# Kernel tuning notes

Measured on AMD Instinct MI355X. Metric: run time of the kernel, lower is better.

## Reference

```python
import jax, jax.numpy as jnp
import numpy as np

ROWS, COLS = 4096, 11008          # out_features, in_features
NCB, CBSIZE, CLEN = 2, 256, 8     # num_codebooks, 2**nbits, in_group_size
RANK = 32
BLOCK = ROWS                      # bolck_size = reference_weight.shape[0]
N_CODES = ROWS * COLS // CLEN     # total number of codebook entries gathered


def setup_inputs() -> dict:
    key = jax.random.key(0)
    k1, k2, k3, k4, k5 = jax.random.split(key, 5)
    codebooks = jax.random.normal(k1, (NCB, CBSIZE, CLEN), dtype=jnp.float32)
    codes = jax.random.randint(k2, (NCB, N_CODES // NCB), 0, CBSIZE, dtype=jnp.int32)
    scales = jax.random.uniform(k3, (COLS, 1), dtype=jnp.float32, minval=0.5, maxval=1.5)
    L = jax.random.normal(k4, (ROWS, RANK), dtype=jnp.float32) * 0.02
    R = jax.random.normal(k5, (RANK, COLS), dtype=jnp.float32) * 0.02
    return {"codebooks": codebooks, "codes": codes, "scales": scales, "L": L, "R": R}


def reference(codebooks, codes, scales, L, R):
    # differentiable_dequantize: per-codebook gather (embedding_bag with 1-elem
    # bags == plain gather), then per-block scale, then reshape back to weight.
    gathered = jax.vmap(lambda cb, c: cb[c])(codebooks, codes)  # (NCB, N/NCB, CLEN)
    blocks = gathered.reshape(-1, BLOCK) * scales               # (COLS, ROWS) * (COLS,1)
    dequant = blocks.reshape(ROWS, COLS)
    # low-rank correction
    return dequant + L @ R
```

## Files before the change

kernel.cpp:

```cpp
#include <hip/hip_runtime.h>

constexpr int kRows  = 4096;
constexpr int kCols  = 11008;
constexpr int kRank  = 32;

constexpr int RT    = 16;
constexpr int CT    = 256;
constexpr int PITCH = 260;

typedef __attribute__((ext_vector_type(8))) short short8;
typedef __attribute__((ext_vector_type(4))) float f32x4;

__device__ __forceinline__ unsigned short bf16_rne(float x) {
    union { float f; unsigned u; } v; v.f = x;
    return (unsigned short)((v.u + 0x7FFFu + ((v.u >> 16) & 1u)) >> 16);
}

__global__ __launch_bounds__(256) void prep(
    const float* __restrict__ Lm,
    const float* __restrict__ Rm,
    unsigned short* __restrict__ Lb,
    unsigned short* __restrict__ Rbt)
{
    const int tid = threadIdx.x;
    const int b   = blockIdx.x;
    if (b < 43) {
        const int j = b * 256 + tid;
        #pragma unroll
        for (int t = 0; t < 4; ++t) {
            short8 o;
            #pragma unroll
            for (int k = 0; k < 8; ++k)
                o[k] = (short)bf16_rne(Rm[(t * 8 + k) * kCols + j]);
            *(short8*)(Rbt + j * kRank + t * 8) = o;
        }
    } else {
        const int t0 = ((b - 43) * 256 + tid) * 8;
        const float4 a0 = *(const float4*)(Lm + t0);
        const float4 a1 = *(const float4*)(Lm + t0 + 4);
        short8 o;
        o[0] = (short)bf16_rne(a0.x); o[1] = (short)bf16_rne(a0.y);
        o[2] = (short)bf16_rne(a0.z); o[3] = (short)bf16_rne(a0.w);
        o[4] = (short)bf16_rne(a1.x); o[5] = (short)bf16_rne(a1.y);
        o[6] = (short)bf16_rne(a1.z); o[7] = (short)bf16_rne(a1.w);
        *(short8*)(Lb + t0) = o;
    }
}

__global__ __launch_bounds__(256, 6) void qw_fused(
    const float* __restrict__ codebooks,
    const int*   __restrict__ codes,
    const float* __restrict__ scales,
    const unsigned short* __restrict__ Lb,
    const unsigned short* __restrict__ Rbt,
    float* __restrict__ outp)
{
    __shared__ __attribute__((aligned(16))) float cb_lds[256 * 8];
    __shared__ __attribute__((aligned(16))) float corr[RT * PITCH];

    const int tid = threadIdx.x;
    const int i0 = blockIdx.y * RT;
    const int j0 = blockIdx.x * CT;

    {
        const int sel = (i0 >= (kRows >> 1)) ? 1 : 0;
        const f32x4* src = (const f32x4*)codebooks + (sel << 9);
        f32x4* dst = (f32x4*)cb_lds;
        #pragma unroll
        for (int t = 0; t < 2; ++t) dst[tid + t * 256] = src[tid + t * 256];
    }

    {
        const int wave = tid >> 6;
        const int lane = tid & 63;
        const int n16  = lane & 15;
        const int q    = lane >> 4;

        const short8 af = *(const short8*)(Lb + (size_t)(i0 + n16) * kRank + (q << 3));

        const unsigned short* bbase =
            Rbt + (size_t)(j0 + (wave << 6) + n16) * kRank + (q << 3);
        short8 bfr[4];
        #pragma unroll
        for (int nt = 0; nt < 4; ++nt)
            bfr[nt] = *(const short8*)(bbase + nt * 16 * kRank);

        const int row_base = q << 2;
        const int cbase    = (wave << 6) + n16;

        #pragma unroll
        for (int nt = 0; nt < 4; ++nt) {
            f32x4 acc = {0.f, 0.f, 0.f, 0.f};
            acc = __builtin_amdgcn_mfma_f32_16x16x32_bf16(af, bfr[nt], acc, 0, 0, 0);
            const int ccol = cbase + nt * 16;
            #pragma unroll
            for (int r = 0; r < 4; ++r)
                corr[(row_base + r) * PITCH + ccol] = acc[r];
        }
    }

    __syncthreads();

    {
        const int lane4 = (tid & 63) << 2;
        const int rbase = tid >> 6;
        #pragma unroll
        for (int p = 0; p < 4; ++p) {
            const int row = rbase + (p << 2);
            const int f = (i0 + row) * kCols + j0 + lane4;
            const int code = codes[f >> 3];
            const float scale = scales[f >> 12];
            const f32x4 w = *(const f32x4*)(cb_lds + (code << 3) + (lane4 & 4));
            const f32x4 c = *(const f32x4*)(corr + row * PITCH + lane4);
            f32x4 o;
            o[0] = w[0] * scale + c[0];
            o[1] = w[1] * scale + c[1];
            o[2] = w[2] * scale + c[2];
            o[3] = w[3] * scale + c[3];
            __builtin_nontemporal_store(o, (f32x4*)(outp + f));
        }
    }
}

extern "C" void kernel_launch(void* const* d_in, const int* in_sizes, int n_in,
                              void* d_out, int out_size, void* d_ws, size_t ws_size,
                              hipStream_t stream) {
    const float* codebooks = (const float*)d_in[0];
    const int*   codes     = (const int*)d_in[1];
    const float* scales    = (const float*)d_in[2];
    const float* Lm        = (const float*)d_in[3];
    const float* Rm        = (const float*)d_in[4];
    float* outp            = (float*)d_out;

    unsigned short* Lb  = (unsigned short*)d_ws;
    unsigned short* Rbt = Lb + kRows * kRank;

    prep<<<dim3(43 + 64), dim3(256), 0, stream>>>(Lm, Rm, Lb, Rbt);

    dim3 grid(kCols / CT, kRows / RT);
    qw_fused<<<grid, dim3(256), 0, stream>>>(codebooks, codes, scales, Lb, Rbt, outp);
}
```

Before: 223.0 us.

## Process several column tiles per block with double-buffered correction and in-kernel L conversion

Each block now handles up to four consecutive 256-column tiles instead of one. The next tile's low-rank correction is computed by MFMA into a second LDS buffer while the current tile is dequantized and stored. The codebook LDS load and L fragment are amortized across tiles, and L is converted to bf16 inside the main kernel, so the prep kernel only transposes R. The grid gets smaller and the occupancy hint of 6 is removed, which can reduce parallelism, and the last column chunk is partial (43 tiles split into chunks of 4).

```diff
diff --git a/kernel.cpp b/kernel.cpp
--- a/kernel.cpp
+++ b/kernel.cpp
@@ -4,9 +4,11 @@
 constexpr int kCols  = 11008;
 constexpr int kRank  = 32;
 
-constexpr int RT    = 16;
-constexpr int CT    = 256;
-constexpr int PITCH = 260;
+constexpr int RT     = 16;
+constexpr int CT     = 256;
+constexpr int PITCH  = 260;
+constexpr int JCHUNK = 4;
+constexpr int NJT    = kCols / CT;
 
 typedef __attribute__((ext_vector_type(8))) short short8;
 typedef __attribute__((ext_vector_type(4))) float f32x4;
@@ -16,94 +18,90 @@
     return (unsigned short)((v.u + 0x7FFFu + ((v.u >> 16) & 1u)) >> 16);
 }
 
-__global__ __launch_bounds__(256) void prep(
-    const float* __restrict__ Lm,
+__global__ __launch_bounds__(256) void prep_r(
     const float* __restrict__ Rm,
-    unsigned short* __restrict__ Lb,
     unsigned short* __restrict__ Rbt)
 {
-    const int tid = threadIdx.x;
-    const int b   = blockIdx.x;
-    if (b < 43) {
-        const int j = b * 256 + tid;
+    const int j = blockIdx.x * 256 + threadIdx.x;
+    #pragma unroll
+    for (int t = 0; t < 4; ++t) {
+        short8 o;
         #pragma unroll
-        for (int t = 0; t < 4; ++t) {
-            short8 o;
-            #pragma unroll
-            for (int k = 0; k < 8; ++k)
-                o[k] = (short)bf16_rne(Rm[(t * 8 + k) * kCols + j]);
-            *(short8*)(Rbt + j * kRank + t * 8) = o;
-        }
-    } else {
-        const int t0 = ((b - 43) * 256 + tid) * 8;
-        const float4 a0 = *(const float4*)(Lm + t0);
-        const float4 a1 = *(const float4*)(Lm + t0 + 4);
-        short8 o;
-        o[0] = (short)bf16_rne(a0.x); o[1] = (short)bf16_rne(a0.y);
-        o[2] = (short)bf16_rne(a0.z); o[3] = (short)bf16_rne(a0.w);
-        o[4] = (short)bf16_rne(a1.x); o[5] = (short)bf16_rne(a1.y);
-        o[6] = (short)bf16_rne(a1.z); o[7] = (short)bf16_rne(a1.w);
-        *(short8*)(Lb + t0) = o;
+        for (int k = 0; k < 8; ++k)
+            o[k] = (short)bf16_rne(Rm[(t * 8 + k) * kCols + j]);
+        *(short8*)(Rbt + j * kRank + t * 8) = o;
     }
 }
 
-__global__ __launch_bounds__(256, 6) void qw_fused(
+__global__ __launch_bounds__(256) void qw_fused(
     const float* __restrict__ codebooks,
     const int*   __restrict__ codes,
     const float* __restrict__ scales,
-    const unsigned short* __restrict__ Lb,
+    const float* __restrict__ Lm,
     const unsigned short* __restrict__ Rbt,
     float* __restrict__ outp)
 {
     __shared__ __attribute__((aligned(16))) float cb_lds[256 * 8];
-    __shared__ __attribute__((aligned(16))) float corr[RT * PITCH];
+    __shared__ __attribute__((aligned(16))) float corr[2][RT * PITCH];
 
-    const int tid = threadIdx.x;
-    const int i0 = blockIdx.y * RT;
-    const int j0 = blockIdx.x * CT;
+    const int tid  = threadIdx.x;
+    const int wave = tid >> 6;
+    const int lane = tid & 63;
+    const int n16  = lane & 15;
+    const int q    = lane >> 4;
+    const int i0   = blockIdx.y * RT;
+    const int jt0  = blockIdx.x * JCHUNK;
+    const int ntiles = (NJT - jt0 < JCHUNK) ? (NJT - jt0) : JCHUNK;
 
     {
         const int sel = (i0 >= (kRows >> 1)) ? 1 : 0;
         const f32x4* src = (const f32x4*)codebooks + (sel << 9);
         f32x4* dst = (f32x4*)cb_lds;
-        #pragma unroll
-        for (int t = 0; t < 2; ++t) dst[tid + t * 256] = src[tid + t * 256];
+        dst[tid]       = src[tid];
+        dst[tid + 256] = src[tid + 256];
     }
 
+    short8 af;
     {
-        const int wave = tid >> 6;
-        const int lane = tid & 63;
-        const int n16  = lane & 15;
-        const int q    = lane >> 4;
+        const float* ap = Lm + (size_t)(i0 + n16) * kRank + (q << 3);
+        const f32x4 a0 = *(const f32x4*)ap;
+        const f32x4 a1 = *(const f32x4*)(ap + 4);
+        af[0] = (short)bf16_rne(a0[0]); af[1] = (short)bf16_rne(a0[1]);
+        af[2] = (short)bf16_rne(a0[2]); af[3] = (short)bf16_rne(a0[3]);
+        af[4] = (short)bf16_rne(a1[0]); af[5] = (short)bf16_rne(a1[1]);
+        af[6] = (short)bf16_rne(a1[2]); af[7] = (short)bf16_rne(a1[3]);
+    }
 
-        const short8 af = *(const short8*)(Lb + (size_t)(i0 + n16) * kRank + (q << 3));
+    const int row_base = q << 2;
+    const int cbase    = (wave << 6) + n16;
 
+    auto compute_corr = [&](int jt, int buf) {
         const unsigned short* bbase =
-            Rbt + (size_t)(j0 + (wave << 6) + n16) * kRank + (q << 3);
-        short8 bfr[4];
-        #pragma unroll
-        for (int nt = 0; nt < 4; ++nt)
-            bfr[nt] = *(const short8*)(bbase + nt * 16 * kRank);
-
-        const int row_base = q << 2;
-        const int cbase    = (wave << 6) + n16;
-
+            Rbt + (size_t)(jt * CT + (wave << 6) + n16) * kRank + (q << 3);
         #pragma unroll
         for (int nt = 0; nt < 4; ++nt) {
+            const short8 bfr = *(const short8*)(bbase + nt * 16 * kRank);
             f32x4 acc = {0.f, 0.f, 0.f, 0.f};
-            acc = __builtin_amdgcn_mfma_f32_16x16x32_bf16(af, bfr[nt], acc, 0, 0, 0);
+            acc = __builtin_amdgcn_mfma_f32_16x16x32_bf16(af, bfr, acc, 0, 0, 0);
             const int ccol = cbase + nt * 16;
             #pragma unroll
             for (int r = 0; r < 4; ++r)
-                corr[(row_base + r) * PITCH + ccol] = acc[r];
+                corr[buf][(row_base + r) * PITCH + ccol] = acc[r];
         }
-    }
+    };
 
-    __syncthreads();
+    compute_corr(jt0, 0);
 
-    {
-        const int lane4 = (tid & 63) << 2;
-        const int rbase = tid >> 6;
+    const int lane4 = lane << 2;
+    const int rbase = wave;
+
+    for (int t = 0; t < ntiles; ++t) {
+        __syncthreads();
+        if (t + 1 < ntiles)
+            compute_corr(jt0 + t + 1, (t + 1) & 1);
+
+        const float* cbuf = corr[t & 1];
+        const int j0 = (jt0 + t) * CT;
         #pragma unroll
         for (int p = 0; p < 4; ++p) {
             const int row = rbase + (p << 2);
@@ -111,7 +109,7 @@
             const int code = codes[f >> 3];
             const float scale = scales[f >> 12];
             const f32x4 w = *(const f32x4*)(cb_lds + (code << 3) + (lane4 & 4));
-            const f32x4 c = *(const f32x4*)(corr + row * PITCH + lane4);
+            const f32x4 c = *(const f32x4*)(cbuf + row * PITCH + lane4);
             f32x4 o;
             o[0] = w[0] * scale + c[0];
             o[1] = w[1] * scale + c[1];
@@ -132,11 +130,10 @@
     const float* Rm        = (const float*)d_in[4];
     float* outp            = (float*)d_out;
 
-    unsigned short* Lb  = (unsigned short*)d_ws;
-    unsigned short* Rbt = Lb + kRows * kRank;
+    unsigned short* Rbt = (unsigned short*)d_ws;
 
-    prep<<<dim3(43 + 64), dim3(256), 0, stream>>>(Lm, Rm, Lb, Rbt);
+    prep_r<<<dim3(43), dim3(256), 0, stream>>>(Rm, Rbt);
 
-    dim3 grid(kCols / CT, kRows / RT);
-    qw_fused<<<grid, dim3(256), 0, stream>>>(codebooks, codes, scales, Lb, Rbt, outp);
+    dim3 grid((NJT + JCHUNK - 1) / JCHUNK, kRows / RT);
+    qw_fused<<<grid, dim3(256), 0, stream>>>(codebooks, codes, scales, Lm, Rbt, outp);
 }
```

New measurement: 232.3 us. +4.2%, slower.
